# Performance work log

Hardware: AMD Instinct MI355X
Metric: run time of the kernel (lower is better)

Reference implementation:

```python
import jax, jax.numpy as jnp
import numpy as np

B, D = 8192, 1024
TEMPERATURE = 0.05
NEG_INF = -9e15


def setup_inputs() -> dict:
    key = jax.random.key(0)
    k1, k2, k3 = jax.random.split(key, 3)
    emb = jax.random.normal(k1, (B, D), dtype=jnp.float32)
    # L2-normalize so sim/temperature is numerically sane (as in real usage)
    emb = emb / jnp.linalg.norm(emb, axis=-1, keepdims=True)
    relations = jax.random.randint(k2, (B,), 0, 128, dtype=jnp.int64)
    is_true_samples = jax.random.bernoulli(k3, 0.5, (B,))
    return {"embeddings": emb, "relations": relations, "is_true_samples": is_true_samples}


def reference(embeddings, relations, is_true_samples):
    b = embeddings.shape[0]
    # [B, B] similarity, diagonal masked to -9e15 as in the original
    sim = jnp.matmul(embeddings, embeddings.T) / TEMPERATURE
    eye = jnp.eye(b, dtype=bool)
    sim = jnp.where(eye, NEG_INF, sim)
    # positive_pairs[i, j] = is_true[i] & is_true[j] & (rel[i] == rel[j]) & (i != j)
    pos = (
        (relations[:, None] == relations[None, :])
        & is_true_samples[:, None]
        & is_true_samples[None, :]
        & ~eye
    )
    exp_sim = jnp.exp(sim)                      # diagonal exp(-9e15) -> 0
    sum_exp = exp_sim.sum(axis=1)               # [B]
    numer = jnp.where(pos, exp_sim, 0.0).sum(axis=1)  # [B]
    has_pos = pos.any(axis=1)                   # [B]
    numer_safe = jnp.where(has_pos, numer, 1.0)
    losses = -jnp.log(numer_safe / (sum_exp + 1e-8))
    n_rows = has_pos.sum()
    loss = jnp.where(
        n_rows > 0,
        jnp.where(has_pos, losses, 0.0).sum() / jnp.maximum(n_rows, 1).astype(losses.dtype),
        jnp.asarray(0.0, dtype=losses.dtype),
    )
    num_positives = n_rows  # rows having at least one positive, as in the original
    return loss, num_positives
```

## Files before the change

### kernel.cpp

```cpp
#include <hip/hip_runtime.h>
#include <hip/hip_bf16.h>
#include <hip/hip_fp8.h>
#include <stdint.h>

#define NB 8192
#define ND 1024
#define SCALE 20.0f
#define PRESCALE 16.0f
#define EXPSCALE (SCALE / (PRESCALE * PRESCALE))

typedef __bf16 bf16x8 __attribute__((ext_vector_type(8)));
typedef float  f32x4  __attribute__((ext_vector_type(4)));
typedef long   lx2    __attribute__((ext_vector_type(2)));

__device__ inline void detect_formats(const void* rel_raw, const void* ist_raw,
                                      int& rel64, int& bmode) {
  const unsigned int* r = (const unsigned int*)rel_raw;
  int is64 = 1;
  for (int i = 1; i < 256; i += 2) {
    if (r[i] != 0u) { is64 = 0; break; }
  }
  rel64 = is64;
  const unsigned int* t = (const unsigned int*)ist_raw;
  bool sawf = false, sawbig = false;
  for (int i = 0; i < 64; ++i) {
    unsigned int w = t[i];
    if (w == 0x3F800000u) sawf = true;
    else if (w > 1u) sawbig = true;
  }
  bmode = sawf ? 2 : (sawbig ? 1 : 0);
}

__device__ inline int decode_key(const void* rel_raw, const void* ist_raw,
                                 int rel64, int bmode, int i) {
  const int* r32 = (const int*)rel_raw;
  int r = rel64 ? r32[2 * i] : r32[i];
  int truth;
  if (bmode == 1)      truth = (((const unsigned char*)ist_raw)[i] != 0);
  else if (bmode == 2) truth = (((const float*)ist_raw)[i] != 0.0f);
  else                 truth = (((const int*)ist_raw)[i] != 0);
  return truth ? r : -1;
}

__device__ inline bf16x8 cvt8(const float4& a, const float4& b) {
  bf16x8 v;
  v[0] = (__bf16)a.x; v[1] = (__bf16)a.y; v[2] = (__bf16)a.z; v[3] = (__bf16)a.w;
  v[4] = (__bf16)b.x; v[5] = (__bf16)b.y; v[6] = (__bf16)b.z; v[7] = (__bf16)b.w;
  return v;
}

__device__ inline unsigned long long cvt8f8(const float4& a, const float4& b) {
  float v[8] = {a.x, a.y, a.z, a.w, b.x, b.y, b.z, b.w};
  unsigned long long pk = 0;
#pragma unroll
  for (int i = 0; i < 8; ++i) {
    __hip_fp8_e4m3 h(v[i] * PRESCALE);
    pk |= (unsigned long long)(unsigned char)h.__x << (8 * i);
  }
  return pk;
}

__global__ void prep_kernel(const float* __restrict__ emb,
                            const void* __restrict__ rel_raw,
                            const void* __restrict__ ist_raw,
                            unsigned char* __restrict__ emb8,
                            float* __restrict__ sum_exp,
                            float* __restrict__ numer,
                            int* __restrict__ key) {
  int tid = blockIdx.x * 256 + threadIdx.x;
  size_t base = (size_t)tid * 8;
  if (base < (size_t)NB * ND) {
    float4 a = *(const float4*)(emb + base);
    float4 b = *(const float4*)(emb + base + 4);
    int u = (int)((base >> 3) & 7);
    size_t dest = (base & ~(size_t)63) | ((size_t)(2 * (u & 3) + (u >> 2)) << 3);
    *(unsigned long long*)(emb8 + dest) = cvt8f8(a, b);
  }
  if (tid < NB) { sum_exp[tid] = 0.f; numer[tid] = 0.f; }
  __shared__ int s_rel64, s_bmode;
  if (blockIdx.x < 32) {
    if (threadIdx.x == 0) {
      int a, b; detect_formats(rel_raw, ist_raw, a, b);
      s_rel64 = a; s_bmode = b;
    }
    __syncthreads();
    int i = blockIdx.x * 256 + threadIdx.x;
    key[i] = decode_key(rel_raw, ist_raw, s_rel64, s_bmode, i);
  }
}

__global__ void prep_small_kernel(const void* __restrict__ rel_raw,
                                  const void* __restrict__ ist_raw,
                                  float* __restrict__ sum_exp,
                                  float* __restrict__ numer,
                                  int* __restrict__ key) {
  int i = blockIdx.x * 256 + threadIdx.x;
  sum_exp[i] = 0.f; numer[i] = 0.f;
  __shared__ int s_rel64, s_bmode;
  if (threadIdx.x == 0) {
    int a, b; detect_formats(rel_raw, ist_raw, a, b);
    s_rel64 = a; s_bmode = b;
  }
  __syncthreads();
  key[i] = decode_key(rel_raw, ist_raw, s_rel64, s_bmode, i);
}


__global__ __launch_bounds__(256, 4)
void gemm_f8v_kernel(const unsigned char* __restrict__ emb8,
                     const int* __restrict__ key,
                     float* __restrict__ sum_exp,
                     float* __restrict__ numer) {
  __shared__ unsigned char sT[3][2][8192];
  __shared__ int keyR[128], keyC[128];

  const int bid = blockIdx.x;
  const int t = (bid & 7) * 260 + (bid >> 3);
  int r = (int)((sqrtf(8.f * (float)t + 1.f) - 1.f) * 0.5f);
  while ((r + 1) * (r + 2) / 2 <= t) ++r;
  while (r * (r + 1) / 2 > t) --r;
  const int bx = r, by = t - r * (r + 1) / 2;
  const bool diag = (bx == by);
  const int rowBase = by * 128, colBase = bx * 128;

  const int tid = threadIdx.x;
  const int wid = tid >> 6;
  const int l   = tid & 63;
  const int wr  = wid >> 1;
  const int wc  = wid & 1;

  const int fragOff = (l & 15) * 64 + (((l >> 4) ^ ((l >> 1) & 3)) * 16);
  const int srow = l >> 2;
  const int scol = (((l & 3) ^ ((l >> 3) & 3)) * 16);

  if (tid < 128) keyR[tid] = key[rowBase + tid];
  else           keyC[tid - 128] = key[colBase + tid - 128];
  asm volatile("" ::: "memory");

  const size_t aOff0 = (size_t)(rowBase + (wid * 2 + 0) * 16 + srow) * ND + scol;
  const size_t aOff1 = (size_t)(rowBase + (wid * 2 + 1) * 16 + srow) * ND + scol;
  const size_t bOff0 = (size_t)(colBase + (wid * 2 + 0) * 16 + srow) * ND + scol;
  const size_t bOff1 = (size_t)(colBase + (wid * 2 + 1) * 16 + srow) * ND + scol;
  const int dst0 = (wid * 2 + 0) * 1024 + l * 16;
  const int dst1 = (wid * 2 + 1) * 1024 + l * 16;

#define STAGE(buf, k0)                                                         \
  do {                                                                         \
    __builtin_amdgcn_global_load_lds(                                          \
        (const __attribute__((address_space(1))) void*)(emb8 + aOff0 + (k0)),  \
        (__attribute__((address_space(3))) void*)&sT[buf][0][dst0], 16, 0, 0); \
    __builtin_amdgcn_global_load_lds(                                          \
        (const __attribute__((address_space(1))) void*)(emb8 + aOff1 + (k0)),  \
        (__attribute__((address_space(3))) void*)&sT[buf][0][dst1], 16, 0, 0); \
    __builtin_amdgcn_global_load_lds(                                          \
        (const __attribute__((address_space(1))) void*)(emb8 + bOff0 + (k0)),  \
        (__attribute__((address_space(3))) void*)&sT[buf][1][dst0], 16, 0, 0); \
    __builtin_amdgcn_global_load_lds(                                          \
        (const __attribute__((address_space(1))) void*)(emb8 + bOff1 + (k0)),  \
        (__attribute__((address_space(3))) void*)&sT[buf][1][dst1], 16, 0, 0); \
  } while (0)

  STAGE(0, 0);

  f32x4 acc[4][4] = {};
  int rb = 0, wb = 1;

#pragma unroll 1
  for (int kt = 0; kt < 16; ++kt) {
    if (kt < 15) {
      STAGE(wb, (kt + 1) * 64);
      asm volatile("s_waitcnt vmcnt(4) lgkmcnt(0)" ::: "memory");
    } else {
      asm volatile("s_waitcnt vmcnt(0) lgkmcnt(0)" ::: "memory");
    }
    __builtin_amdgcn_s_barrier();
    asm volatile("" ::: "memory");

    const unsigned char* cA = &sT[rb][0][0];
    const unsigned char* cB = &sT[rb][1][0];
    lx2 a2[4], b2[4];
#pragma unroll
    for (int m = 0; m < 4; ++m)
      a2[m] = *(const lx2*)&cA[(wr * 4 + m) * 1024 + fragOff];
#pragma unroll
    for (int n = 0; n < 4; ++n)
      b2[n] = *(const lx2*)&cB[(wc * 4 + n) * 1024 + fragOff];
    __builtin_amdgcn_s_setprio(1);
#pragma unroll
    for (int m = 0; m < 4; ++m)
#pragma unroll
      for (int n = 0; n < 4; ++n)
        acc[m][n] = __builtin_amdgcn_mfma_f32_16x16x32_fp8_fp8(a2[m][0], b2[n][0], acc[m][n], 0, 0, 0);
#pragma unroll
    for (int m = 0; m < 4; ++m)
#pragma unroll
      for (int n = 0; n < 4; ++n)
        acc[m][n] = __builtin_amdgcn_mfma_f32_16x16x32_fp8_fp8(a2[m][1], b2[n][1], acc[m][n], 0, 0, 0);
    __builtin_amdgcn_s_setprio(0);

    rb = (rb == 2) ? 0 : rb + 1;
    wb = (wb == 2) ? 0 : wb + 1;
  }
#undef STAGE

  float cse[4] = {0.f, 0.f, 0.f, 0.f};
  float cnu[4] = {0.f, 0.f, 0.f, 0.f};
#pragma unroll
  for (int m = 0; m < 4; ++m) {
#pragma unroll
    for (int r4 = 0; r4 < 4; ++r4) {
      int li = wr * 64 + m * 16 + (l >> 4) * 4 + r4;
      int gi = rowBase + li;
      int krow = keyR[li];
      float se = 0.f, nu = 0.f;
#pragma unroll
      for (int n = 0; n < 4; ++n) {
        int lj = wc * 64 + n * 16 + (l & 15);
        int gj = colBase + lj;
        float e = __expf(acc[m][n][r4] * EXPSCALE);
        if (gi == gj) e = 0.f;
        bool match = (krow >= 0) && (krow == keyC[lj]);
        se += e;
        if (match) nu += e;
        if (!diag) {
          cse[n] += e;
          if (match) cnu[n] += e;
        }
      }
#pragma unroll
      for (int off = 8; off; off >>= 1) {
        se += __shfl_xor(se, off, 16);
        nu += __shfl_xor(nu, off, 16);
      }
      if ((l & 15) == 0) {
        atomicAdd(&sum_exp[gi], se);
        if (nu != 0.f) atomicAdd(&numer[gi], nu);
      }
    }
  }
  if (!diag) {
#pragma unroll
    for (int n = 0; n < 4; ++n) {
      cse[n] += __shfl_xor(cse[n], 16);
      cse[n] += __shfl_xor(cse[n], 32);
      cnu[n] += __shfl_xor(cnu[n], 16);
      cnu[n] += __shfl_xor(cnu[n], 32);
    }
    if (l < 16) {
#pragma unroll
      for (int n = 0; n < 4; ++n) {
        int gj = colBase + wc * 64 + n * 16 + l;
        atomicAdd(&sum_exp[gj], cse[n]);
        if (cnu[n] != 0.f) atomicAdd(&numer[gj], cnu[n]);
      }
    }
  }
}

__global__ __launch_bounds__(256, 4)
void gemm_fused_f32_kernel(const float* __restrict__ embF,
                           const int* __restrict__ key,
                           float* __restrict__ sum_exp,
                           float* __restrict__ numer) {
  __shared__ __bf16 sA[128 * 64];
  __shared__ __bf16 sB[128 * 64];
  __shared__ int keyR[128], keyC[128];

  const int t = blockIdx.x;
  int r = (int)((sqrtf(8.f * (float)t + 1.f) - 1.f) * 0.5f);
  while ((r + 1) * (r + 2) / 2 <= t) ++r;
  while (r * (r + 1) / 2 > t) --r;
  const int bx = r;
  const int by = t - r * (r + 1) / 2;
  const bool diag = (bx == by);

  const int tid = threadIdx.x;
  const int wid = tid >> 6;
  const int l   = tid & 63;
  const int wr  = wid >> 1;
  const int wc  = wid & 1;
  const int rowBase = by * 128;
  const int colBase = bx * 128;

  if (tid < 128) keyR[tid] = key[rowBase + tid];
  else           keyC[tid - 128] = key[colBase + tid - 128];

  f32x4 acc[4][4] = {};

  for (int k0 = 0; k0 < ND; k0 += 64) {
    __syncthreads();
#pragma unroll
    for (int c = 0; c < 4; ++c) {
      int chunk = tid + c * 256;
      int row = chunk >> 3;
      int ko  = (chunk & 7) * 8;
      const float* gfa = embF + (size_t)(rowBase + row) * ND + k0 + ko;
      const float* gfb = embF + (size_t)(colBase + row) * ND + k0 + ko;
      float4 a0 = *(const float4*)gfa;
      float4 a1 = *(const float4*)(gfa + 4);
      float4 b0 = *(const float4*)gfb;
      float4 b1 = *(const float4*)(gfb + 4);
      *(bf16x8*)&sA[row * 64 + ko] = cvt8(a0, a1);
      *(bf16x8*)&sB[row * 64 + ko] = cvt8(b0, b1);
    }
    __syncthreads();

#pragma unroll
    for (int kk = 0; kk < 2; ++kk) {
      bf16x8 af[4], bfr[4];
#pragma unroll
      for (int m = 0; m < 4; ++m)
        af[m] = *(const bf16x8*)&sA[(wr * 64 + m * 16 + (l & 15)) * 64 + kk * 32 + (l >> 4) * 8];
#pragma unroll
      for (int n = 0; n < 4; ++n)
        bfr[n] = *(const bf16x8*)&sB[(wc * 64 + n * 16 + (l & 15)) * 64 + kk * 32 + (l >> 4) * 8];
#pragma unroll
      for (int m = 0; m < 4; ++m)
#pragma unroll
        for (int n = 0; n < 4; ++n)
          acc[m][n] = __builtin_amdgcn_mfma_f32_16x16x32_bf16(af[m], bfr[n], acc[m][n], 0, 0, 0);
    }
  }

  float cse[4] = {0.f, 0.f, 0.f, 0.f};
  float cnu[4] = {0.f, 0.f, 0.f, 0.f};
#pragma unroll
  for (int m = 0; m < 4; ++m) {
#pragma unroll
    for (int r4 = 0; r4 < 4; ++r4) {
      int li = wr * 64 + m * 16 + (l >> 4) * 4 + r4;
      int gi = rowBase + li;
      int krow = keyR[li];
      float se = 0.f, nu = 0.f;
#pragma unroll
      for (int n = 0; n < 4; ++n) {
        int lj = wc * 64 + n * 16 + (l & 15);
        int gj = colBase + lj;
        float e = __expf(acc[m][n][r4] * SCALE);
        if (gi == gj) e = 0.f;
        bool match = (krow >= 0) && (krow == keyC[lj]);
        se += e;
        if (match) nu += e;
        if (!diag) {
          cse[n] += e;
          if (match) cnu[n] += e;
        }
      }
#pragma unroll
      for (int off = 8; off; off >>= 1) {
        se += __shfl_xor(se, off, 16);
        nu += __shfl_xor(nu, off, 16);
      }
      if ((l & 15) == 0) {
        atomicAdd(&sum_exp[gi], se);
        if (nu != 0.f) atomicAdd(&numer[gi], nu);
      }
    }
  }
  if (!diag) {
#pragma unroll
    for (int n = 0; n < 4; ++n) {
      cse[n] += __shfl_xor(cse[n], 16);
      cse[n] += __shfl_xor(cse[n], 32);
      cnu[n] += __shfl_xor(cnu[n], 16);
      cnu[n] += __shfl_xor(cnu[n], 32);
    }
    if (l < 16) {
#pragma unroll
      for (int n = 0; n < 4; ++n) {
        int gj = colBase + wc * 64 + n * 16 + l;
        atomicAdd(&sum_exp[gj], cse[n]);
        if (cnu[n] != 0.f) atomicAdd(&numer[gj], cnu[n]);
      }
    }
  }
}

__global__ void finalize_kernel(const float* __restrict__ sum_exp,
                                const float* __restrict__ numer,
                                const int* __restrict__ key,
                                float* __restrict__ out) {
  __shared__ int cnt[128];
  __shared__ float wsum[16];
  __shared__ int wcnt[16];
  int tid = threadIdx.x;
  if (tid < 128) cnt[tid] = 0;
  __syncthreads();
  for (int i = tid; i < NB; i += 1024) {
    int k = key[i];
    if (k >= 0) atomicAdd(&cnt[k], 1);
  }
  __syncthreads();
  float ls = 0.f; int np = 0;
  for (int i = tid; i < NB; i += 1024) {
    int k = key[i];
    if (k >= 0 && cnt[k] >= 2) {
      np++;
      ls += logf(sum_exp[i] + 1e-8f) - logf(numer[i]);
    }
  }
  for (int off = 32; off; off >>= 1) {
    ls += __shfl_down(ls, off, 64);
    np += __shfl_down(np, off, 64);
  }
  int w = tid >> 6;
  if ((tid & 63) == 0) { wsum[w] = ls; wcnt[w] = np; }
  __syncthreads();
  if (tid == 0) {
    float s = 0.f; int n = 0;
    for (int i = 0; i < 16; ++i) { s += wsum[i]; n += wcnt[i]; }
    out[0] = (n > 0) ? (s / (float)n) : 0.f;
    out[1] = (float)n;
  }
}

#define NT128 64
#define NTRI128 (NT128 * (NT128 + 1) / 2)

extern "C" void kernel_launch(void* const* d_in, const int* in_sizes, int n_in,
                              void* d_out, int out_size, void* d_ws, size_t ws_size,
                              hipStream_t stream) {
  const float* emb = (const float*)d_in[0];
  const void* rel  = d_in[1];
  const void* ist  = d_in[2];
  float* out = (float*)d_out;

  const size_t emb8Bytes = (size_t)NB * ND;
  const size_t smallBytes = (size_t)NB * 4 * 3;

  char* ws = (char*)d_ws;
  if (ws_size >= emb8Bytes + smallBytes) {
    unsigned char* emb8 = (unsigned char*)ws;
    float* sum_exp = (float*)(ws + emb8Bytes);
    float* numer   = sum_exp + NB;
    int*   key     = (int*)(numer + NB);
    prep_kernel<<<4096, 256, 0, stream>>>(emb, rel, ist, emb8, sum_exp, numer, key);
    gemm_f8v_kernel<<<NTRI128, 256, 0, stream>>>(emb8, key, sum_exp, numer);
    finalize_kernel<<<1, 1024, 0, stream>>>(sum_exp, numer, key, out);
  } else {
    float* sum_exp = (float*)ws;
    float* numer   = sum_exp + NB;
    int*   key     = (int*)(numer + NB);
    prep_small_kernel<<<32, 256, 0, stream>>>(rel, ist, sum_exp, numer, key);
    gemm_fused_f32_kernel<<<NTRI128, 256, 0, stream>>>(emb, key, sum_exp, numer);
    finalize_kernel<<<1, 1024, 0, stream>>>(sum_exp, numer, key, out);
  }
}
```

Baseline: 100.5 us.

## Switch FP8 GEMM to 32x32x64 scaled MFMA with unit scales

```diff
diff --git a/kernel.cpp b/kernel.cpp
--- a/kernel.cpp
+++ b/kernel.cpp
@@ -11,7 +11,11 @@
 
 typedef __bf16 bf16x8 __attribute__((ext_vector_type(8)));
 typedef float  f32x4  __attribute__((ext_vector_type(4)));
-typedef long   lx2    __attribute__((ext_vector_type(2)));
+typedef float  f32x16 __attribute__((ext_vector_type(16)));
+typedef int    i32x4  __attribute__((ext_vector_type(4)));
+typedef int    i32x8  __attribute__((ext_vector_type(8)));
+
+#define SC1 0x7F7F7F7F
 
 __device__ inline void detect_formats(const void* rel_raw, const void* ist_raw,
                                       int& rel64, int& bmode) {
@@ -72,9 +76,7 @@
   if (base < (size_t)NB * ND) {
     float4 a = *(const float4*)(emb + base);
     float4 b = *(const float4*)(emb + base + 4);
-    int u = (int)((base >> 3) & 7);
-    size_t dest = (base & ~(size_t)63) | ((size_t)(2 * (u & 3) + (u >> 2)) << 3);
-    *(unsigned long long*)(emb8 + dest) = cvt8f8(a, b);
+    *(unsigned long long*)(emb8 + base) = cvt8f8(a, b);
   }
   if (tid < NB) { sum_exp[tid] = 0.f; numer[tid] = 0.f; }
   __shared__ int s_rel64, s_bmode;
@@ -107,10 +109,10 @@
 
 
 __global__ __launch_bounds__(256, 4)
-void gemm_f8v_kernel(const unsigned char* __restrict__ emb8,
-                     const int* __restrict__ key,
-                     float* __restrict__ sum_exp,
-                     float* __restrict__ numer) {
+void gemm_mx_kernel(const unsigned char* __restrict__ emb8,
+                    const int* __restrict__ key,
+                    float* __restrict__ sum_exp,
+                    float* __restrict__ numer) {
   __shared__ unsigned char sT[3][2][8192];
   __shared__ int keyR[128], keyC[128];
 
@@ -128,8 +130,24 @@
   const int l   = tid & 63;
   const int wr  = wid >> 1;
   const int wc  = wid & 1;
-
-  const int fragOff = (l & 15) * 64 + (((l >> 4) ^ ((l >> 1) & 3)) * 16);
+  const int la  = l & 31;
+  const int h2  = (l >> 5) << 1;
+
+  int aOffL[2][2], bOffL[2][2];
+#pragma unroll
+  for (int i = 0; i < 2; ++i) {
+    int rr = wr * 64 + i * 32 + la;
+    int rbyte = ((rr >> 4) << 10) + ((rr & 15) << 6);
+    int X = (rr >> 1) & 3;
+    aOffL[i][0] = rbyte + ((h2 ^ X) << 4);
+    aOffL[i][1] = rbyte + (((h2 + 1) ^ X) << 4);
+    int cc = wc * 64 + i * 32 + la;
+    int cbyte = ((cc >> 4) << 10) + ((cc & 15) << 6);
+    int Xc = (cc >> 1) & 3;
+    bOffL[i][0] = cbyte + ((h2 ^ Xc) << 4);
+    bOffL[i][1] = cbyte + (((h2 + 1) ^ Xc) << 4);
+  }
+
   const int srow = l >> 2;
   const int scol = (((l & 3) ^ ((l >> 3) & 3)) * 16);
 
@@ -162,7 +180,7 @@
 
   STAGE(0, 0);
 
-  f32x4 acc[4][4] = {};
+  f32x16 acc32[2][2] = {};
   int rb = 0, wb = 1;
 
 #pragma unroll 1
@@ -178,24 +196,26 @@
 
     const unsigned char* cA = &sT[rb][0][0];
     const unsigned char* cB = &sT[rb][1][0];
-    lx2 a2[4], b2[4];
-#pragma unroll
-    for (int m = 0; m < 4; ++m)
-      a2[m] = *(const lx2*)&cA[(wr * 4 + m) * 1024 + fragOff];
-#pragma unroll
-    for (int n = 0; n < 4; ++n)
-      b2[n] = *(const lx2*)&cB[(wc * 4 + n) * 1024 + fragOff];
+    i32x8 a8[2], b8[2];
+#pragma unroll
+    for (int i = 0; i < 2; ++i) {
+      i32x4 lo = *(const i32x4*)&cA[aOffL[i][0]];
+      i32x4 hi = *(const i32x4*)&cA[aOffL[i][1]];
+      a8[i] = __builtin_shufflevector(lo, hi, 0, 1, 2, 3, 4, 5, 6, 7);
+    }
+#pragma unroll
+    for (int j = 0; j < 2; ++j) {
+      i32x4 lo = *(const i32x4*)&cB[bOffL[j][0]];
+      i32x4 hi = *(const i32x4*)&cB[bOffL[j][1]];
+      b8[j] = __builtin_shufflevector(lo, hi, 0, 1, 2, 3, 4, 5, 6, 7);
+    }
     __builtin_amdgcn_s_setprio(1);
 #pragma unroll
-    for (int m = 0; m < 4; ++m)
-#pragma unroll
-      for (int n = 0; n < 4; ++n)
-        acc[m][n] = __builtin_amdgcn_mfma_f32_16x16x32_fp8_fp8(a2[m][0], b2[n][0], acc[m][n], 0, 0, 0);
-#pragma unroll
-    for (int m = 0; m < 4; ++m)
-#pragma unroll
-      for (int n = 0; n < 4; ++n)
-        acc[m][n] = __builtin_amdgcn_mfma_f32_16x16x32_fp8_fp8(a2[m][1], b2[n][1], acc[m][n], 0, 0, 0);
+    for (int i = 0; i < 2; ++i)
+#pragma unroll
+      for (int j = 0; j < 2; ++j)
+        acc32[i][j] = __builtin_amdgcn_mfma_scale_f32_32x32x64_f8f6f4(
+            a8[i], b8[j], acc32[i][j], 0, 0, 0, SC1, 0, SC1);
     __builtin_amdgcn_s_setprio(0);
 
     rb = (rb == 2) ? 0 : rb + 1;
@@ -203,36 +223,37 @@
   }
 #undef STAGE
 
-  float cse[4] = {0.f, 0.f, 0.f, 0.f};
-  float cnu[4] = {0.f, 0.f, 0.f, 0.f};
-#pragma unroll
-  for (int m = 0; m < 4; ++m) {
-#pragma unroll
-    for (int r4 = 0; r4 < 4; ++r4) {
-      int li = wr * 64 + m * 16 + (l >> 4) * 4 + r4;
+  float csum[2] = {0.f, 0.f};
+  float cnum[2] = {0.f, 0.f};
+#pragma unroll
+  for (int i = 0; i < 2; ++i) {
+#pragma unroll
+    for (int reg = 0; reg < 16; ++reg) {
+      int row = (reg & 3) + 8 * (reg >> 2) + 4 * (l >> 5);
+      int li = wr * 64 + i * 32 + row;
       int gi = rowBase + li;
       int krow = keyR[li];
       float se = 0.f, nu = 0.f;
 #pragma unroll
-      for (int n = 0; n < 4; ++n) {
-        int lj = wc * 64 + n * 16 + (l & 15);
+      for (int j = 0; j < 2; ++j) {
+        int lj = wc * 64 + j * 32 + la;
         int gj = colBase + lj;
-        float e = __expf(acc[m][n][r4] * EXPSCALE);
+        float e = __expf(acc32[i][j][reg] * EXPSCALE);
         if (gi == gj) e = 0.f;
         bool match = (krow >= 0) && (krow == keyC[lj]);
         se += e;
         if (match) nu += e;
         if (!diag) {
-          cse[n] += e;
-          if (match) cnu[n] += e;
+          csum[j] += e;
+          if (match) cnum[j] += e;
         }
       }
 #pragma unroll
-      for (int off = 8; off; off >>= 1) {
-        se += __shfl_xor(se, off, 16);
-        nu += __shfl_xor(nu, off, 16);
-      }
-      if ((l & 15) == 0) {
+      for (int off = 1; off < 32; off <<= 1) {
+        se += __shfl_xor(se, off);
+        nu += __shfl_xor(nu, off);
+      }
+      if (la == 0) {
         atomicAdd(&sum_exp[gi], se);
         if (nu != 0.f) atomicAdd(&numer[gi], nu);
       }
@@ -240,18 +261,16 @@
   }
   if (!diag) {
 #pragma unroll
-    for (int n = 0; n < 4; ++n) {
-      cse[n] += __shfl_xor(cse[n], 16);
-      cse[n] += __shfl_xor(cse[n], 32);
-      cnu[n] += __shfl_xor(cnu[n], 16);
-      cnu[n] += __shfl_xor(cnu[n], 32);
-    }
-    if (l < 16) {
-#pragma unroll
-      for (int n = 0; n < 4; ++n) {
-        int gj = colBase + wc * 64 + n * 16 + l;
-        atomicAdd(&sum_exp[gj], cse[n]);
-        if (cnu[n] != 0.f) atomicAdd(&numer[gj], cnu[n]);
+    for (int j = 0; j < 2; ++j) {
+      csum[j] += __shfl_xor(csum[j], 32);
+      cnum[j] += __shfl_xor(cnum[j], 32);
+    }
+    if (l < 32) {
+#pragma unroll
+      for (int j = 0; j < 2; ++j) {
+        int gj = colBase + wc * 64 + j * 32 + l;
+        atomicAdd(&sum_exp[gj], csum[j]);
+        if (cnum[j] != 0.f) atomicAdd(&numer[gj], cnum[j]);
       }
     }
   }
@@ -435,7 +454,7 @@
     float* numer   = sum_exp + NB;
     int*   key     = (int*)(numer + NB);
     prep_kernel<<<4096, 256, 0, stream>>>(emb, rel, ist, emb8, sum_exp, numer, key);
-    gemm_f8v_kernel<<<NTRI128, 256, 0, stream>>>(emb8, key, sum_exp, numer);
+    gemm_mx_kernel<<<NTRI128, 256, 0, stream>>>(emb8, key, sum_exp, numer);
     finalize_kernel<<<1, 1024, 0, stream>>>(sum_exp, numer, key, out);
   } else {
     float* sum_exp = (float*)ws;
```

Result: slower. 111.6 us (+11.1%).
